# Kernel optimization log

Measured on AMD Instinct MI355X. Metric: run time of the kernel, lower is better.

## Reference

```python
import jax, jax.numpy as jnp
import numpy as np

N_KNOTS = 10
NEXPERTS = 1
NC = 8
STEP = 1.0 / (N_KNOTS - 1.0)
BN_EPS = 1e-5


def _spline_matrix(n, step):
    # natural cubic spline second-derivative solve matrix (precalc in torch code)
    mat = 4.0 * np.eye(n - 2)
    np.fill_diagonal(mat[1:, :-1], 1.0)
    np.fill_diagonal(mat[:-1, 1:], 1.0)
    A = 6.0 * np.linalg.inv(mat) / step ** 2
    z = np.zeros((1, n - 2))
    A = np.vstack([z, A, z])                      # [n, n-2]
    B = np.zeros((n - 2, n))
    np.fill_diagonal(B, 1.0)
    np.fill_diagonal(B[:, 1:], -2.0)
    np.fill_diagonal(B[:, 2:], 1.0)
    return jnp.asarray(A @ B, dtype=jnp.float32)  # [n, n]


def _conv(x, w, b, stride=2):
    y = jax.lax.conv_general_dilated(x, w, (stride, stride), 'VALID',
                                     dimension_numbers=('NCHW', 'OIHW', 'NCHW'))
    return y + b[None, :, None, None]


def _bn(x, g, be):
    # training-mode batchnorm (module default)
    m = x.mean(axis=(0, 2, 3), keepdims=True)
    v = x.var(axis=(0, 2, 3), keepdims=True)
    return g[None, :, None, None] * (x - m) * jax.lax.rsqrt(v + BN_EPS) + be[None, :, None, None]


def _interpolate(ys, mat):
    # ys: [..., n] -> cubic coeffs a,b,c,d each [..., n-1]
    h = STEP
    M = jnp.einsum('ij,...j->...i', mat, ys)
    a = (M[..., 1:] - M[..., :-1]) / (6.0 * h)
    b = M[..., :-1] / 2.0
    c = (ys[..., 1:] - ys[..., :-1]) / h - (M[..., 1:] + 2.0 * M[..., :-1]) * (h / 6.0)
    d = ys[..., :-1]
    return a, b, c, d


def _apply(coeffs, x):
    # coeffs: 4-tuple each [..., n-1]; x: [..., P] with matching leading dims
    a, b, c, d = coeffs
    xi = jnp.clip(jnp.floor(x / STEP), 0.0, N_KNOTS - 2.0)
    xf = x - xi * STEP
    idx = xi.astype(jnp.int32)
    ag = jnp.take_along_axis(a, idx, axis=-1)
    bg = jnp.take_along_axis(b, idx, axis=-1)
    cg = jnp.take_along_axis(c, idx, axis=-1)
    dg = jnp.take_along_axis(d, idx, axis=-1)
    return ((ag * xf + bg) * xf + cg) * xf + dg


def forward(x, w1, b1, w2, b2, g2, be2, w3, b3, g3, be3, w4, b4, g4, be4,
            w5, b5, g5, be5, fc1_w, fc1_b, fc2_w, fc2_b):
    B, C, H, W = x.shape
    small = x if (H, W) == (256, 256) else jax.image.resize(x, (B, C, 256, 256), 'bilinear')
    h = jax.nn.relu(_conv(small, w1, b1))
    h = _bn(jax.nn.relu(_conv(h, w2, b2)), g2, be2)
    h = _bn(jax.nn.relu(_conv(h, w3, b3)), g3, be3)
    h = _bn(jax.nn.relu(_conv(h, w4, b4)), g4, be4)
    h = _bn(jax.nn.relu(_conv(h, w5, b5)), g5, be5)   # [B, 16nc, 7, 7]
    h = h.mean(axis=(2, 3))                            # avgpool 7 -> [B, 16nc]
    h = jax.nn.relu(h @ fc1_w.T + fc1_b)
    ys = (h @ fc2_w.T + fc2_b).reshape(B, NEXPERTS, 3, N_KNOTS)
    identity = jnp.arange(N_KNOTS, dtype=jnp.float32) / (N_KNOTS - 1.0)
    ysn = ys + identity                                # residual spline
    mat = _spline_matrix(N_KNOTS, STEP)
    coeffs = _interpolate(ysn, mat)                    # each [B,E,3,n-1]
    # per-pixel spline eval at original resolution
    px = jnp.broadcast_to(x.reshape(B, 1, 3, H * W), (B, NEXPERTS, 3, H * W))
    out = _apply(coeffs, px).reshape(B, NEXPERTS, 3, H, W)
    out = jnp.transpose(out, (1, 0, 2, 3, 4))          # [E,B,3,H,W]
    # spline curves sampled at xs = arange(0,1,1/255) (255 points; detached in torch)
    xs = jnp.arange(0.0, 1.0, 1.0 / 255.0, dtype=jnp.float32)
    xs_b = jnp.broadcast_to(xs, (B, NEXPERTS, 3, xs.shape[0]))
    splines = jnp.transpose(_apply(coeffs, xs_b), (1, 0, 2, 3))  # [E,B,3,255]
    return out, splines


def setup_inputs() -> dict:
    key = jax.random.key(0)
    ks = jax.random.split(key, 16)
    n, nc, E = N_KNOTS, NC, NEXPERTS
    d = {}
    d['x'] = jax.random.uniform(ks[0], (8, 3, 1024, 1024), dtype=jnp.float32)
    d['w1'] = jax.random.normal(ks[1], (nc, 3, 3, 3), jnp.float32) * 0.1
    d['b1'] = jnp.zeros((nc,), jnp.float32)
    chans = [nc, 2 * nc, 4 * nc, 8 * nc, 16 * nc]
    for i, (ci, co) in enumerate(zip(chans[:-1], chans[1:]), start=2):
        d[f'w{i}'] = jax.random.normal(ks[i], (co, ci, 3, 3), jnp.float32) * 0.1
        d[f'b{i}'] = jnp.zeros((co,), jnp.float32)
        d[f'g{i}'] = jnp.ones((co,), jnp.float32)
        d[f'be{i}'] = jnp.zeros((co,), jnp.float32)
    d['fc1_w'] = jax.random.normal(ks[10], (16 * nc, 16 * nc), jnp.float32) * 0.05
    d['fc1_b'] = jnp.zeros((16 * nc,), jnp.float32)
    d['fc2_w'] = jax.random.normal(ks[11], (3 * n * E, 16 * nc), jnp.float32) * 0.05
    d['fc2_b'] = jnp.zeros((3 * n * E,), jnp.float32)
    return d


def reference(x, w1, b1, w2, b2, g2, be2, w3, b3, g3, be3, w4, b4, g4, be4,
              w5, b5, g5, be5, fc1_w, fc1_b, fc2_w, fc2_b):
    return forward(x, w1, b1, w2, b2, g2, be2, w3, b3, g3, be3, w4, b4, g4, be4,
                   w5, b5, g5, be5, fc1_w, fc1_b, fc2_w, fc2_b)
```

## Files before the change

kernel.cpp:

```cpp
#include <hip/hip_runtime.h>

#define SPLINE_OFF 25165824
#define STEP_F (1.0f/9.0f)

typedef float f32x4 __attribute__((ext_vector_type(4)));

__global__ __launch_bounds__(256) void resize_k(const float* __restrict__ x,
                                                float* __restrict__ sm) {
    __shared__ float vs[2][1024];
    const int blk = blockIdx.x;
    const int plane = blk >> 7;
    const int orA = (blk & 127) * 2;
    const int t = threadIdx.x;

    const float W[8] = {0.125f,0.375f,0.625f,0.875f,0.875f,0.625f,0.375f,0.125f};
    const float* p = x + (size_t)plane * 1048576 + t * 4;
    const int rA = 4 * orA - 2;

    float a0x=0.f,a0y=0.f,a0z=0.f,a0w=0.f;
    float a1x=0.f,a1y=0.f,a1z=0.f,a1w=0.f;

    if (rA >= 0 && rA + 11 <= 1023) {
        #pragma unroll
        for (int k = 0; k < 12; k++) {
            const float4 v = *(const float4*)(p + (size_t)(rA + k) * 1024);
            if (k < 8) {
                const float w = W[k] * 0.25f;
                a0x = fmaf(v.x, w, a0x); a0y = fmaf(v.y, w, a0y);
                a0z = fmaf(v.z, w, a0z); a0w = fmaf(v.w, w, a0w);
            }
            if (k >= 4) {
                const float w = W[k - 4] * 0.25f;
                a1x = fmaf(v.x, w, a1x); a1y = fmaf(v.y, w, a1y);
                a1z = fmaf(v.z, w, a1z); a1w = fmaf(v.w, w, a1w);
            }
        }
    } else {
        #pragma unroll
        for (int o = 0; o < 2; o++) {
            const int r0 = 4 * (orA + o) - 2;
            float bx=0.f,by=0.f,bz=0.f,bw=0.f,wsum=0.f;
            #pragma unroll
            for (int k = 0; k < 8; k++) {
                const int r = r0 + k;
                if (r >= 0 && r < 1024) {
                    const float4 v = *(const float4*)(p + (size_t)r * 1024);
                    bx = fmaf(v.x, W[k], bx); by = fmaf(v.y, W[k], by);
                    bz = fmaf(v.z, W[k], bz); bw = fmaf(v.w, W[k], bw);
                    wsum += W[k];
                }
            }
            const float inv = 1.f / wsum;
            if (o == 0) { a0x=bx*inv; a0y=by*inv; a0z=bz*inv; a0w=bw*inv; }
            else        { a1x=bx*inv; a1y=by*inv; a1z=bz*inv; a1w=bw*inv; }
        }
    }
    vs[0][4*t+0]=a0x; vs[0][4*t+1]=a0y; vs[0][4*t+2]=a0z; vs[0][4*t+3]=a0w;
    vs[1][4*t+0]=a1x; vs[1][4*t+1]=a1y; vs[1][4*t+2]=a1z; vs[1][4*t+3]=a1w;
    __syncthreads();

    const int c0 = 4 * t - 2;
    #pragma unroll
    for (int o = 0; o < 2; o++) {
        float acc = 0.f;
        if (c0 >= 0 && c0 + 7 <= 1023) {
            #pragma unroll
            for (int k = 0; k < 8; k++)
                acc = fmaf(vs[o][c0 + k], W[k] * 0.25f, acc);
        } else {
            float wsum = 0.f;
            #pragma unroll
            for (int k = 0; k < 8; k++) {
                const int c = c0 + k;
                if (c >= 0 && c < 1024) { acc = fmaf(vs[o][c], W[k], acc); wsum += W[k]; }
            }
            acc /= wsum;
        }
        sm[((size_t)plane * 256 + orA + o) * 256 + t] = acc;
    }
}

__global__ __launch_bounds__(256) void c1c2_k(
    const float* __restrict__ sm,
    const float* __restrict__ w1, const float* __restrict__ b1,
    const float* __restrict__ w2, const float* __restrict__ b2,
    float* __restrict__ h2, float* __restrict__ pS2, float* __restrict__ pQ2)
{
    __shared__ float smT[3 * 1225];
    __shared__ float c1T[8 * 289];
    __shared__ float w1s[216];
    __shared__ float w2s[1152];
    __shared__ float bs[24];

    const int tile = blockIdx.x;
    const int b    = blockIdx.y;
    const int tx = tile & 7, ty = tile >> 3;
    const int R0 = ty * 8, C0 = tx * 8;
    const int t = threadIdx.x;

    if (t < 216) w1s[t] = w1[t];
    for (int i = t; i < 1152; i += 256) w2s[i] = w2[i];
    if (t < 8) bs[t] = b1[t];
    else if (t < 24) bs[t] = b2[t - 8];

    const int r0 = 4 * R0, c0 = 4 * C0;
    for (int i = t; i < 3675; i += 256) {
        const int ch = i / 1225, rem = i - ch * 1225;
        const int r = rem / 35, c = rem - r * 35;
        const int gr = r0 + r, gc = c0 + c;
        float v = 0.f;
        if (gr < 256 && gc < 256)
            v = sm[((size_t)(b * 3 + ch) << 16) + (gr << 8) + gc];
        smT[i] = v;
    }
    __syncthreads();

    for (int i = t; i < 2312; i += 256) {
        const int co = i / 289, pp = i - co * 289;
        const int r = pp / 17, c = pp - r * 17;
        float acc = bs[co];
        #pragma unroll
        for (int ch = 0; ch < 3; ch++) {
            const float* sp = &smT[ch * 1225 + (2 * r) * 35 + 2 * c];
            const float* wp = &w1s[co * 27 + ch * 9];
            #pragma unroll
            for (int kh = 0; kh < 3; kh++) {
                acc = fmaf(sp[kh * 35 + 0], wp[kh * 3 + 0], acc);
                acc = fmaf(sp[kh * 35 + 1], wp[kh * 3 + 1], acc);
                acc = fmaf(sp[kh * 35 + 2], wp[kh * 3 + 2], acc);
            }
        }
        c1T[i] = fmaxf(acc, 0.f);
    }
    __syncthreads();

    const int px = t & 63, cog = t >> 6;
    const int pr = px >> 3, pc = px & 7;
    const bool valid = (R0 + pr < 63) && (C0 + pc < 63);
    float vals[4];
    #pragma unroll
    for (int k = 0; k < 4; k++) {
        const int co = cog * 4 + k;
        float acc = bs[8 + co];
        #pragma unroll
        for (int ci = 0; ci < 8; ci++) {
            const float* cp = &c1T[ci * 289 + (2 * pr) * 17 + 2 * pc];
            const float* wp = &w2s[co * 72 + ci * 9];
            #pragma unroll
            for (int kh = 0; kh < 3; kh++) {
                acc = fmaf(cp[kh * 17 + 0], wp[kh * 3 + 0], acc);
                acc = fmaf(cp[kh * 17 + 1], wp[kh * 3 + 1], acc);
                acc = fmaf(cp[kh * 17 + 2], wp[kh * 3 + 2], acc);
            }
        }
        const float v = valid ? fmaxf(acc, 0.f) : 0.f;
        vals[k] = v;
        if (valid)
            h2[(size_t)(b * 16 + co) * 3969 + (R0 + pr) * 63 + (C0 + pc)] = v;
    }
    #pragma unroll
    for (int k = 0; k < 4; k++) {
        float s = vals[k], q = vals[k] * vals[k];
        #pragma unroll
        for (int off = 32; off > 0; off >>= 1) {
            s += __shfl_down(s, off);
            q += __shfl_down(q, off);
        }
        if (px == 0) {
            const int co = cog * 4 + k;
            pS2[(b * 16 + co) * 64 + tile] = s;
            pQ2[(b * 16 + co) * 64 + tile] = q;
        }
    }
}

template<int CIN, int COUT, int INW, int OUTW, int CISPLIT, int PIX,
         int NTPREV, int NTOUT, bool INBN, bool STATS, bool WRITE>
__global__ __launch_bounds__(PIX * CISPLIT) void conv_k(
    const float* __restrict__ in, const float* __restrict__ w,
    const float* __restrict__ bias,
    const float* __restrict__ gam, const float* __restrict__ be,
    const float* __restrict__ pS, const float* __restrict__ pQ, float invN,
    float* __restrict__ out,
    float* __restrict__ pSo, float* __restrict__ pQo)
{
    constexpr int BLOCK = PIX * CISPLIT;
    constexpr int CPS = CIN / CISPLIT;
    constexpr int COG = COUT / 2;

    __shared__ float wsm[2][CIN * 9];
    __shared__ float scs[CIN], shs[CIN];
    __shared__ float wrow[2][CIN];
    __shared__ float cadd[2];
    __shared__ float part[CISPLIT][PIX][2];
    __shared__ float red[2][2][PIX / 64];
    __shared__ float sredS[BLOCK], sredQ[BLOCK];

    const int tid = threadIdx.x;
    const int p   = tid & (PIX - 1);
    const int cs  = tid / PIX;
    const int bc  = blockIdx.y;
    const int b   = bc / COG;
    const int co0 = (bc % COG) * 2;

    if constexpr (INBN) {
        constexpr int GRP = BLOCK / CIN;
        constexpr int TERMS = 8 * NTPREV;
        const int ci = tid % CIN;
        const int gi = tid / CIN;
        float s = 0.f, q = 0.f;
        for (int j = gi; j < TERMS; j += GRP) {
            const int bb = j / NTPREV, tl = j - bb * NTPREV;
            const int a = (bb * CIN + ci) * NTPREV + tl;
            s += pS[a]; q += pQ[a];
        }
        sredS[gi * CIN + ci] = s;
        sredQ[gi * CIN + ci] = q;
        __syncthreads();
        if (tid < CIN) {
            float ts = 0.f, tq = 0.f;
            #pragma unroll
            for (int g2 = 0; g2 < GRP; g2++) {
                ts += sredS[g2 * CIN + tid];
                tq += sredQ[g2 * CIN + tid];
            }
            const float m = ts * invN;
            const float v = tq * invN - m * m;
            const float sc = gam[tid] * rsqrtf(v + 1e-5f);
            scs[tid] = sc;
            shs[tid] = be[tid] - m * sc;
        }
        __syncthreads();
    }

    for (int i = tid; i < 2 * CIN * 9; i += BLOCK) {
        const int n = i / (CIN * 9), r = i - n * (CIN * 9), ci = r / 9;
        const float wv = w[(co0 + n) * CIN * 9 + r];
        wsm[n][r] = INBN ? wv * scs[ci] : wv;
    }
    if constexpr (INBN) {
        for (int i = tid; i < 2 * CIN; i += BLOCK) {
            const int n = i / CIN, ci = i - n * CIN;
            const float* wp = w + ((co0 + n) * CIN + ci) * 9;
            float s = 0.f;
            #pragma unroll
            for (int k = 0; k < 9; k++) s += wp[k];
            wrow[n][ci] = s;
        }
    }
    __syncthreads();
    if (tid < 2) {
        float c = bias[co0 + tid];
        if constexpr (INBN) {
            for (int ci = 0; ci < CIN; ci++) c = fmaf(wrow[tid][ci], shs[ci], c);
        }
        cadd[tid] = c;
    }
    __syncthreads();

    const int npix = OUTW * OUTW;
    const int pg = blockIdx.x * PIX + p;
    float a0 = 0.f, a1 = 0.f;
    if (pg < npix) {
        const int oh = pg / OUTW, ow = pg - oh * OUTW;
        const float* ib = in + ((size_t)(b * CIN) + cs * CPS) * (INW * INW)
                             + (size_t)(2 * oh) * INW + 2 * ow;
        #pragma unroll 4
        for (int ci = 0; ci < CPS; ci++) {
            const float* ip = ib + (size_t)ci * (INW * INW);
            const int cw = (cs * CPS + ci) * 9;
            #pragma unroll
            for (int kh = 0; kh < 3; kh++) {
                const float* r = ip + kh * INW;
                #pragma unroll
                for (int kw = 0; kw < 3; kw++) {
                    const float xv = r[kw];
                    a0 = fmaf(xv, wsm[0][cw + kh * 3 + kw], a0);
                    a1 = fmaf(xv, wsm[1][cw + kh * 3 + kw], a1);
                }
            }
        }
    }

    float v0 = 0.f, v1 = 0.f;
    if constexpr (CISPLIT > 1) {
        part[cs][p][0] = a0; part[cs][p][1] = a1;
        __syncthreads();
    }
    if (cs == 0) {
        float s0 = a0, s1 = a1;
        if constexpr (CISPLIT > 1) {
            #pragma unroll
            for (int q = 1; q < CISPLIT; q++) { s0 += part[q][p][0]; s1 += part[q][p][1]; }
        }
        if (pg < npix) {
            v0 = fmaxf(s0 + cadd[0], 0.f);
            v1 = fmaxf(s1 + cadd[1], 0.f);
            if constexpr (WRITE) {
                out[(size_t)(b * COUT + co0) * npix + pg] = v0;
                out[(size_t)(b * COUT + co0 + 1) * npix + pg] = v1;
            }
        }
    }

    if constexpr (STATS) {
        if (cs == 0) {
            float sA = v0, qA = v0 * v0, sB = v1, qB = v1 * v1;
            #pragma unroll
            for (int off = 32; off > 0; off >>= 1) {
                sA += __shfl_down(sA, off); qA += __shfl_down(qA, off);
                sB += __shfl_down(sB, off); qB += __shfl_down(qB, off);
            }
            if ((tid & 63) == 0) {
                red[0][0][tid >> 6] = sA; red[0][1][tid >> 6] = qA;
                red[1][0][tid >> 6] = sB; red[1][1][tid >> 6] = qB;
            }
        }
        __syncthreads();
        if (tid == 0) {
            float tsA = 0.f, tqA = 0.f, tsB = 0.f, tqB = 0.f;
            #pragma unroll
            for (int i = 0; i < PIX / 64; i++) {
                tsA += red[0][0][i]; tqA += red[0][1][i];
                tsB += red[1][0][i]; tqB += red[1][1][i];
            }
            pSo[(b * COUT + co0) * NTOUT + blockIdx.x] = tsA;
            pQo[(b * COUT + co0) * NTOUT + blockIdx.x] = tqA;
            pSo[(b * COUT + co0 + 1) * NTOUT + blockIdx.x] = tsB;
            pQo[(b * COUT + co0 + 1) * NTOUT + blockIdx.x] = tqB;
        }
    }
}

__global__ __launch_bounds__(256) void fc_spline_k(
    const float* __restrict__ pS5, const float* __restrict__ pQ5,
    const float* __restrict__ g5, const float* __restrict__ be5,
    const float* __restrict__ fc1w, const float* __restrict__ fc1b,
    const float* __restrict__ fc2w, const float* __restrict__ fc2b,
    float* __restrict__ coeff_out, float* __restrict__ splines_out)
{
    __shared__ float sc5[128], sh5[128];
    __shared__ float h[1024];
    __shared__ float h1v[1024];
    __shared__ float ysn[240];
    __shared__ float coef[24][36];

    const int t = threadIdx.x;

    if (t < 128) {
        float s = 0.f, q = 0.f;
        #pragma unroll
        for (int b = 0; b < 8; b++) { s += pS5[b * 128 + t]; q += pQ5[b * 128 + t]; }
        float m = s * (1.f / 392.f);
        float v = q * (1.f / 392.f) - m * m;
        float sc = g5[t] * rsqrtf(v + 1e-5f);
        sc5[t] = sc;
        sh5[t] = be5[t] - m * sc;
    }
    __syncthreads();

    for (int i = t; i < 1024; i += 256) {
        int c = i & 127;
        h[i] = fmaf(sc5[c], pS5[i] * (1.f / 49.f), sh5[c]);
    }
    __syncthreads();

    for (int i = t; i < 1024; i += 256) {
        int b = i >> 7, j = i & 127;
        float acc = fc1b[j];
        for (int c = 0; c < 128; c++)
            acc = fmaf(h[(b << 7) + c], fc1w[(j << 7) + c], acc);
        h1v[i] = fmaxf(acc, 0.f);
    }
    __syncthreads();

    if (t < 240) {
        int b = t / 30, k = t % 30;
        float acc = fc2b[k];
        for (int j = 0; j < 128; j++)
            acc = fmaf(h1v[(b << 7) + j], fc2w[(k << 7) + j], acc);
        ysn[t] = acc + (float)(k % 10) * STEP_F;
    }
    __syncthreads();

    if (t < 24) {
        float y[10];
        #pragma unroll
        for (int i = 0; i < 10; i++) y[i] = ysn[t * 10 + i];
        float rhs[9], cp[9], dp[9];
        #pragma unroll
        for (int i = 1; i <= 8; i++)
            rhs[i] = 486.f * (y[i - 1] - 2.f * y[i] + y[i + 1]);
        cp[1] = 0.25f; dp[1] = rhs[1] * 0.25f;
        #pragma unroll
        for (int i = 2; i <= 8; i++) {
            float m = 1.f / (4.f - cp[i - 1]);
            cp[i] = m;
            dp[i] = (rhs[i] - dp[i - 1]) * m;
        }
        float M[10];
        M[0] = 0.f; M[9] = 0.f;
        M[8] = dp[8];
        #pragma unroll
        for (int i = 7; i >= 1; i--) M[i] = dp[i] - cp[i] * M[i + 1];
        #pragma unroll
        for (int i = 0; i < 9; i++) {
            float a = (M[i + 1] - M[i]) * 1.5f;
            float bb = M[i] * 0.5f;
            float cc = (y[i + 1] - y[i]) * 9.f - (M[i + 1] + 2.f * M[i]) * (STEP_F / 6.f);
            float dd = y[i];
            coef[t][i] = a; coef[t][9 + i] = bb; coef[t][18 + i] = cc; coef[t][27 + i] = dd;
            coeff_out[t * 36 + i] = a;
            coeff_out[t * 36 + 9 + i] = bb;
            coeff_out[t * 36 + 18 + i] = cc;
            coeff_out[t * 36 + 27 + i] = dd;
        }
    }
    __syncthreads();

    for (int i = t; i < 24 * 255; i += 256) {
        int bc = i / 255, k = i - bc * 255;
        float xv = (float)k * (1.0f / 255.0f);
        float xi = floorf(xv * 9.0f);
        xi = fminf(fmaxf(xi, 0.f), 8.f);
        int ix = (int)xi;
        float xf = xv - xi * STEP_F;
        const float* cf = coef[bc];
        splines_out[i] = fmaf(fmaf(fmaf(cf[ix], xf, cf[9 + ix]), xf, cf[18 + ix]), xf, cf[27 + ix]);
    }
}

__global__ __launch_bounds__(256) void apply_k(const float* __restrict__ x,
                                               const float* __restrict__ coeff,
                                               float* __restrict__ out)
{
    __shared__ float cf[36];
    const int blk = blockIdx.x;
    const int plane = blk >> 10;
    const int t = threadIdx.x;
    if (t < 36) cf[t] = coeff[plane * 36 + t];
    __syncthreads();

    size_t base = (size_t)blk * 1024 + (size_t)t * 4;
    float4 v = *(const float4*)(x + base);
    f32x4 o;
    #pragma unroll
    for (int k = 0; k < 4; k++) {
        float xv = (k == 0) ? v.x : (k == 1) ? v.y : (k == 2) ? v.z : v.w;
        float xi = floorf(xv * 9.0f);
        xi = fminf(fmaxf(xi, 0.f), 8.f);
        int ix = (int)xi;
        float xf = xv - xi * STEP_F;
        o[k] = fmaf(fmaf(fmaf(cf[ix], xf, cf[9 + ix]), xf, cf[18 + ix]), xf, cf[27 + ix]);
    }
    __builtin_nontemporal_store(o, (f32x4*)(out + base));
}

extern "C" void kernel_launch(void* const* d_in, const int* in_sizes, int n_in,
                              void* d_out, int out_size, void* d_ws, size_t ws_size,
                              hipStream_t stream) {
    (void)in_sizes; (void)n_in; (void)out_size; (void)ws_size;

    const float* x    = (const float*)d_in[0];
    const float* w1   = (const float*)d_in[1];
    const float* b1   = (const float*)d_in[2];
    const float* w2   = (const float*)d_in[3];
    const float* b2   = (const float*)d_in[4];
    const float* g2   = (const float*)d_in[5];
    const float* be2  = (const float*)d_in[6];
    const float* w3   = (const float*)d_in[7];
    const float* b3   = (const float*)d_in[8];
    const float* g3   = (const float*)d_in[9];
    const float* be3  = (const float*)d_in[10];
    const float* w4   = (const float*)d_in[11];
    const float* b4   = (const float*)d_in[12];
    const float* g4   = (const float*)d_in[13];
    const float* be4  = (const float*)d_in[14];
    const float* w5   = (const float*)d_in[15];
    const float* b5   = (const float*)d_in[16];
    const float* g5   = (const float*)d_in[17];
    const float* be5  = (const float*)d_in[18];
    const float* fc1w = (const float*)d_in[19];
    const float* fc1b = (const float*)d_in[20];
    const float* fc2w = (const float*)d_in[21];
    const float* fc2b = (const float*)d_in[22];

    float* out = (float*)d_out;
    float* wsf = (float*)d_ws;

    float* pS2 = wsf + 0;
    float* pQ2 = wsf + 8192;
    float* pS3 = wsf + 16384;
    float* pQ3 = wsf + 17408;
    float* pS4 = wsf + 18432;
    float* pQ4 = wsf + 18944;
    float* pS5 = wsf + 19456;
    float* pQ5 = wsf + 20480;
    float* coeff = wsf + 21504;

    float* sm  = out;
    float* h2  = out + 1572864;
    float* h3  = out + 2080896;
    float* h4  = out + 2326912;

    resize_k<<<3072, 256, 0, stream>>>(x, sm);

    c1c2_k<<<dim3(64, 8), 256, 0, stream>>>(sm, w1, b1, w2, b2, h2, pS2, pQ2);

    conv_k<16, 32, 63, 31, 2, 256, 64, 4, true, true, true>
        <<<dim3(4, 128), 512, 0, stream>>>(h2, w3, b3, g2, be2,
                                           pS2, pQ2, 1.0f / 31752.0f,
                                           h3, pS3, pQ3);
    conv_k<32, 64, 31, 15, 4, 256, 4, 1, true, true, true>
        <<<dim3(1, 256), 1024, 0, stream>>>(h3, w4, b4, g3, be3,
                                            pS3, pQ3, 1.0f / 7688.0f,
                                            h4, pS4, pQ4);
    conv_k<64, 128, 15, 7, 8, 64, 1, 1, true, true, false>
        <<<dim3(1, 512), 512, 0, stream>>>(h4, w5, b5, g4, be4,
                                           pS4, pQ4, 1.0f / 1800.0f,
                                           nullptr, pS5, pQ5);

    fc_spline_k<<<1, 256, 0, stream>>>(pS5, pQ5, g5, be5,
                                       fc1w, fc1b, fc2w, fc2b,
                                       coeff, out + SPLINE_OFF);

    apply_k<<<24576, 256, 0, stream>>>(x, coeff, out);
}
```

Baseline: 145.1 us.

## Restructure pipeline: split c1c2, fuse conv5 with FC/spline via atomic last-block

Result: faster. 130.5 us (median of 2 runs) (-10.0%).

```diff
diff --git a/kernel.cpp b/kernel.cpp
--- a/kernel.cpp
+++ b/kernel.cpp
@@ -6,38 +6,44 @@
 typedef float f32x4 __attribute__((ext_vector_type(4)));
 
 __global__ __launch_bounds__(256) void resize_k(const float* __restrict__ x,
-                                                float* __restrict__ sm) {
-    __shared__ float vs[2][1024];
+                                                float* __restrict__ sm,
+                                                unsigned* __restrict__ ctr) {
+    __shared__ float vs[4][1024];
     const int blk = blockIdx.x;
-    const int plane = blk >> 7;
-    const int orA = (blk & 127) * 2;
+    const int plane = blk >> 6;
+    const int orA = (blk & 63) * 4;
     const int t = threadIdx.x;
+    if (blk == 0 && t == 0) ctr[0] = 0u;
 
     const float W[8] = {0.125f,0.375f,0.625f,0.875f,0.875f,0.625f,0.375f,0.125f};
     const float* p = x + (size_t)plane * 1048576 + t * 4;
-    const int rA = 4 * orA - 2;
-
-    float a0x=0.f,a0y=0.f,a0z=0.f,a0w=0.f;
-    float a1x=0.f,a1y=0.f,a1z=0.f,a1w=0.f;
-
-    if (rA >= 0 && rA + 11 <= 1023) {
-        #pragma unroll
-        for (int k = 0; k < 12; k++) {
-            const float4 v = *(const float4*)(p + (size_t)(rA + k) * 1024);
-            if (k < 8) {
-                const float w = W[k] * 0.25f;
-                a0x = fmaf(v.x, w, a0x); a0y = fmaf(v.y, w, a0y);
-                a0z = fmaf(v.z, w, a0z); a0w = fmaf(v.w, w, a0w);
-            }
-            if (k >= 4) {
-                const float w = W[k - 4] * 0.25f;
-                a1x = fmaf(v.x, w, a1x); a1y = fmaf(v.y, w, a1y);
-                a1z = fmaf(v.z, w, a1z); a1w = fmaf(v.w, w, a1w);
+    const int rb = 4 * orA - 2;
+
+    float acc[4][4];
+    #pragma unroll
+    for (int o = 0; o < 4; o++)
+        #pragma unroll
+        for (int c = 0; c < 4; c++) acc[o][c] = 0.f;
+
+    if (rb >= 0 && rb + 19 <= 1023) {
+        #pragma unroll
+        for (int k = 0; k < 20; k++) {
+            const float4 v = *(const float4*)(p + (size_t)(rb + k) * 1024);
+            #pragma unroll
+            for (int o = 0; o < 4; o++) {
+                const int j = k - 4 * o;
+                if (j >= 0 && j < 8) {
+                    const float w = W[j] * 0.25f;
+                    acc[o][0] = fmaf(v.x, w, acc[o][0]);
+                    acc[o][1] = fmaf(v.y, w, acc[o][1]);
+                    acc[o][2] = fmaf(v.z, w, acc[o][2]);
+                    acc[o][3] = fmaf(v.w, w, acc[o][3]);
+                }
             }
         }
     } else {
         #pragma unroll
-        for (int o = 0; o < 2; o++) {
+        for (int o = 0; o < 4; o++) {
             const int r0 = 4 * (orA + o) - 2;
             float bx=0.f,by=0.f,bz=0.f,bw=0.f,wsum=0.f;
             #pragma unroll
@@ -51,126 +57,34 @@
                 }
             }
             const float inv = 1.f / wsum;
-            if (o == 0) { a0x=bx*inv; a0y=by*inv; a0z=bz*inv; a0w=bw*inv; }
-            else        { a1x=bx*inv; a1y=by*inv; a1z=bz*inv; a1w=bw*inv; }
-        }
-    }
-    vs[0][4*t+0]=a0x; vs[0][4*t+1]=a0y; vs[0][4*t+2]=a0z; vs[0][4*t+3]=a0w;
-    vs[1][4*t+0]=a1x; vs[1][4*t+1]=a1y; vs[1][4*t+2]=a1z; vs[1][4*t+3]=a1w;
+            acc[o][0]=bx*inv; acc[o][1]=by*inv; acc[o][2]=bz*inv; acc[o][3]=bw*inv;
+        }
+    }
+    #pragma unroll
+    for (int o = 0; o < 4; o++) {
+        vs[o][4*t+0]=acc[o][0]; vs[o][4*t+1]=acc[o][1];
+        vs[o][4*t+2]=acc[o][2]; vs[o][4*t+3]=acc[o][3];
+    }
     __syncthreads();
 
     const int c0 = 4 * t - 2;
     #pragma unroll
-    for (int o = 0; o < 2; o++) {
-        float acc = 0.f;
+    for (int o = 0; o < 4; o++) {
+        float a = 0.f;
         if (c0 >= 0 && c0 + 7 <= 1023) {
             #pragma unroll
             for (int k = 0; k < 8; k++)
-                acc = fmaf(vs[o][c0 + k], W[k] * 0.25f, acc);
+                a = fmaf(vs[o][c0 + k], W[k] * 0.25f, a);
         } else {
             float wsum = 0.f;
             #pragma unroll
             for (int k = 0; k < 8; k++) {
                 const int c = c0 + k;
-                if (c >= 0 && c < 1024) { acc = fmaf(vs[o][c], W[k], acc); wsum += W[k]; }
-            }
-            acc /= wsum;
-        }
-        sm[((size_t)plane * 256 + orA + o) * 256 + t] = acc;
-    }
-}
-
-__global__ __launch_bounds__(256) void c1c2_k(
-    const float* __restrict__ sm,
-    const float* __restrict__ w1, const float* __restrict__ b1,
-    const float* __restrict__ w2, const float* __restrict__ b2,
-    float* __restrict__ h2, float* __restrict__ pS2, float* __restrict__ pQ2)
-{
-    __shared__ float smT[3 * 1225];
-    __shared__ float c1T[8 * 289];
-    __shared__ float w1s[216];
-    __shared__ float w2s[1152];
-    __shared__ float bs[24];
-
-    const int tile = blockIdx.x;
-    const int b    = blockIdx.y;
-    const int tx = tile & 7, ty = tile >> 3;
-    const int R0 = ty * 8, C0 = tx * 8;
-    const int t = threadIdx.x;
-
-    if (t < 216) w1s[t] = w1[t];
-    for (int i = t; i < 1152; i += 256) w2s[i] = w2[i];
-    if (t < 8) bs[t] = b1[t];
-    else if (t < 24) bs[t] = b2[t - 8];
-
-    const int r0 = 4 * R0, c0 = 4 * C0;
-    for (int i = t; i < 3675; i += 256) {
-        const int ch = i / 1225, rem = i - ch * 1225;
-        const int r = rem / 35, c = rem - r * 35;
-        const int gr = r0 + r, gc = c0 + c;
-        float v = 0.f;
-        if (gr < 256 && gc < 256)
-            v = sm[((size_t)(b * 3 + ch) << 16) + (gr << 8) + gc];
-        smT[i] = v;
-    }
-    __syncthreads();
-
-    for (int i = t; i < 2312; i += 256) {
-        const int co = i / 289, pp = i - co * 289;
-        const int r = pp / 17, c = pp - r * 17;
-        float acc = bs[co];
-        #pragma unroll
-        for (int ch = 0; ch < 3; ch++) {
-            const float* sp = &smT[ch * 1225 + (2 * r) * 35 + 2 * c];
-            const float* wp = &w1s[co * 27 + ch * 9];
-            #pragma unroll
-            for (int kh = 0; kh < 3; kh++) {
-                acc = fmaf(sp[kh * 35 + 0], wp[kh * 3 + 0], acc);
-                acc = fmaf(sp[kh * 35 + 1], wp[kh * 3 + 1], acc);
-                acc = fmaf(sp[kh * 35 + 2], wp[kh * 3 + 2], acc);
-            }
-        }
-        c1T[i] = fmaxf(acc, 0.f);
-    }
-    __syncthreads();
-
-    const int px = t & 63, cog = t >> 6;
-    const int pr = px >> 3, pc = px & 7;
-    const bool valid = (R0 + pr < 63) && (C0 + pc < 63);
-    float vals[4];
-    #pragma unroll
-    for (int k = 0; k < 4; k++) {
-        const int co = cog * 4 + k;
-        float acc = bs[8 + co];
-        #pragma unroll
-        for (int ci = 0; ci < 8; ci++) {
-            const float* cp = &c1T[ci * 289 + (2 * pr) * 17 + 2 * pc];
-            const float* wp = &w2s[co * 72 + ci * 9];
-            #pragma unroll
-            for (int kh = 0; kh < 3; kh++) {
-                acc = fmaf(cp[kh * 17 + 0], wp[kh * 3 + 0], acc);
-                acc = fmaf(cp[kh * 17 + 1], wp[kh * 3 + 1], acc);
-                acc = fmaf(cp[kh * 17 + 2], wp[kh * 3 + 2], acc);
-            }
-        }
-        const float v = valid ? fmaxf(acc, 0.f) : 0.f;
-        vals[k] = v;
-        if (valid)
-            h2[(size_t)(b * 16 + co) * 3969 + (R0 + pr) * 63 + (C0 + pc)] = v;
-    }
-    #pragma unroll
-    for (int k = 0; k < 4; k++) {
-        float s = vals[k], q = vals[k] * vals[k];
-        #pragma unroll
-        for (int off = 32; off > 0; off >>= 1) {
-            s += __shfl_down(s, off);
-            q += __shfl_down(q, off);
-        }
-        if (px == 0) {
-            const int co = cog * 4 + k;
-            pS2[(b * 16 + co) * 64 + tile] = s;
-            pQ2[(b * 16 + co) * 64 + tile] = q;
-        }
+                if (c >= 0 && c < 1024) { a = fmaf(vs[o][c], W[k], a); wsum += W[k]; }
+            }
+            a /= wsum;
+        }
+        sm[((size_t)plane * 256 + orA + o) * 256 + t] = a;
     }
 }
 
@@ -332,61 +246,188 @@
     }
 }
 
-__global__ __launch_bounds__(256) void fc_spline_k(
-    const float* __restrict__ pS5, const float* __restrict__ pQ5,
+__global__ __launch_bounds__(256) void conv5fc_k(
+    const float* __restrict__ in, const float* __restrict__ w,
+    const float* __restrict__ bias,
+    const float* __restrict__ gam, const float* __restrict__ be,
+    const float* __restrict__ pS, const float* __restrict__ pQ,
+    float* __restrict__ pS5, float* __restrict__ pQ5,
     const float* __restrict__ g5, const float* __restrict__ be5,
     const float* __restrict__ fc1w, const float* __restrict__ fc1b,
     const float* __restrict__ fc2w, const float* __restrict__ fc2b,
-    float* __restrict__ coeff_out, float* __restrict__ splines_out)
+    float* __restrict__ coeff_out, float* __restrict__ splines_out,
+    unsigned* __restrict__ ctr)
 {
-    __shared__ float sc5[128], sh5[128];
-    __shared__ float h[1024];
-    __shared__ float h1v[1024];
-    __shared__ float ysn[240];
-    __shared__ float coef[24][36];
-
-    const int t = threadIdx.x;
-
+    constexpr int CIN = 64, COUT = 128, INW = 15, OUTW = 7;
+    constexpr int CISPLIT = 4, PIX = 64, BLOCK = 256;
+    constexpr int CPS = CIN / CISPLIT;
+    constexpr int COG = COUT / 2;
+    const float invN = 1.0f / 1800.0f;
+
+    __shared__ float wsm[2][CIN * 9];
+    __shared__ float scs[CIN], shs[CIN];
+    __shared__ float wrow[2][CIN];
+    __shared__ float cadd[2];
+    __shared__ float part[CISPLIT][PIX][2];
+    __shared__ float sredS[BLOCK], sredQ[BLOCK];
+    __shared__ unsigned lastFlag;
+    __shared__ float fsc5[128], fsh5[128];
+    __shared__ float fch[1024], fh1[1024];
+    __shared__ float fysn[240];
+    __shared__ float fcoef[24][36];
+
+    const int tid = threadIdx.x;
+    const int p   = tid & (PIX - 1);
+    const int cs  = tid / PIX;
+    const int bc  = blockIdx.x;
+    const int b   = bc / COG;
+    const int co0 = (bc % COG) * 2;
+
+    {
+        constexpr int GRP = BLOCK / CIN;
+        const int ci = tid % CIN;
+        const int gi = tid / CIN;
+        float s = 0.f, q = 0.f;
+        for (int j = gi; j < 8; j += GRP) {
+            const int a = j * CIN + ci;
+            s += pS[a]; q += pQ[a];
+        }
+        sredS[gi * CIN + ci] = s;
+        sredQ[gi * CIN + ci] = q;
+        __syncthreads();
+        if (tid < CIN) {
+            float ts = 0.f, tq = 0.f;
+            #pragma unroll
+            for (int g2 = 0; g2 < GRP; g2++) {
+                ts += sredS[g2 * CIN + tid];
+                tq += sredQ[g2 * CIN + tid];
+            }
+            const float m = ts * invN;
+            const float v = tq * invN - m * m;
+            const float sc = gam[tid] * rsqrtf(v + 1e-5f);
+            scs[tid] = sc;
+            shs[tid] = be[tid] - m * sc;
+        }
+        __syncthreads();
+    }
+
+    for (int i = tid; i < 2 * CIN * 9; i += BLOCK) {
+        const int n = i / (CIN * 9), r = i - n * (CIN * 9), ci = r / 9;
+        wsm[n][r] = w[(co0 + n) * CIN * 9 + r] * scs[ci];
+    }
+    for (int i = tid; i < 2 * CIN; i += BLOCK) {
+        const int n = i / CIN, ci = i - n * CIN;
+        const float* wp = w + ((co0 + n) * CIN + ci) * 9;
+        float s = 0.f;
+        #pragma unroll
+        for (int k = 0; k < 9; k++) s += wp[k];
+        wrow[n][ci] = s;
+    }
+    __syncthreads();
+    if (tid < 2) {
+        float c = bias[co0 + tid];
+        for (int ci = 0; ci < CIN; ci++) c = fmaf(wrow[tid][ci], shs[ci], c);
+        cadd[tid] = c;
+    }
+    __syncthreads();
+
+    float a0 = 0.f, a1 = 0.f;
+    if (p < 49) {
+        const int oh = p / OUTW, ow = p - oh * OUTW;
+        const float* ib = in + ((size_t)(b * CIN) + cs * CPS) * (INW * INW)
+                             + (size_t)(2 * oh) * INW + 2 * ow;
+        #pragma unroll 4
+        for (int ci = 0; ci < CPS; ci++) {
+            const float* ip = ib + (size_t)ci * (INW * INW);
+            const int cw = (cs * CPS + ci) * 9;
+            #pragma unroll
+            for (int kh = 0; kh < 3; kh++) {
+                const float* r = ip + kh * INW;
+                #pragma unroll
+                for (int kw = 0; kw < 3; kw++) {
+                    const float xv = r[kw];
+                    a0 = fmaf(xv, wsm[0][cw + kh * 3 + kw], a0);
+                    a1 = fmaf(xv, wsm[1][cw + kh * 3 + kw], a1);
+                }
+            }
+        }
+    }
+
+    part[cs][p][0] = a0; part[cs][p][1] = a1;
+    __syncthreads();
+    if (cs == 0) {
+        float s0 = a0 + part[1][p][0] + part[2][p][0] + part[3][p][0];
+        float s1 = a1 + part[1][p][1] + part[2][p][1] + part[3][p][1];
+        float v0 = 0.f, v1 = 0.f;
+        if (p < 49) {
+            v0 = fmaxf(s0 + cadd[0], 0.f);
+            v1 = fmaxf(s1 + cadd[1], 0.f);
+        }
+        float sA = v0, qA = v0 * v0, sB = v1, qB = v1 * v1;
+        #pragma unroll
+        for (int off = 32; off > 0; off >>= 1) {
+            sA += __shfl_down(sA, off); qA += __shfl_down(qA, off);
+            sB += __shfl_down(sB, off); qB += __shfl_down(qB, off);
+        }
+        if (p == 0) {
+            pS5[b * COUT + co0] = sA;
+            pQ5[b * COUT + co0] = qA;
+            pS5[b * COUT + co0 + 1] = sB;
+            pQ5[b * COUT + co0 + 1] = qB;
+        }
+    }
+    __syncthreads();
+
+    if (tid == 0) {
+        __threadfence();
+        unsigned old = atomicAdd(ctr, 1u);
+        lastFlag = (old == 511u) ? 1u : 0u;
+    }
+    __syncthreads();
+    if (lastFlag == 0u) return;
+    __threadfence();
+
+    const int t = tid;
     if (t < 128) {
-        float s = 0.f, q = 0.f;
-        #pragma unroll
-        for (int b = 0; b < 8; b++) { s += pS5[b * 128 + t]; q += pQ5[b * 128 + t]; }
-        float m = s * (1.f / 392.f);
-        float v = q * (1.f / 392.f) - m * m;
+        float sv = 0.f, qv = 0.f;
+        #pragma unroll
+        for (int bb = 0; bb < 8; bb++) { sv += pS5[bb * 128 + t]; qv += pQ5[bb * 128 + t]; }
+        float m = sv * (1.f / 392.f);
+        float v = qv * (1.f / 392.f) - m * m;
         float sc = g5[t] * rsqrtf(v + 1e-5f);
-        sc5[t] = sc;
-        sh5[t] = be5[t] - m * sc;
+        fsc5[t] = sc;
+        fsh5[t] = be5[t] - m * sc;
     }
     __syncthreads();
 
     for (int i = t; i < 1024; i += 256) {
         int c = i & 127;
-        h[i] = fmaf(sc5[c], pS5[i] * (1.f / 49.f), sh5[c]);
+        fch[i] = fmaf(fsc5[c], pS5[i] * (1.f / 49.f), fsh5[c]);
     }
     __syncthreads();
 
     for (int i = t; i < 1024; i += 256) {
-        int b = i >> 7, j = i & 127;
+        int bb = i >> 7, j = i & 127;
         float acc = fc1b[j];
         for (int c = 0; c < 128; c++)
-            acc = fmaf(h[(b << 7) + c], fc1w[(j << 7) + c], acc);
-        h1v[i] = fmaxf(acc, 0.f);
+            acc = fmaf(fch[(bb << 7) + c], fc1w[(j << 7) + c], acc);
+        fh1[i] = fmaxf(acc, 0.f);
     }
     __syncthreads();
 
     if (t < 240) {
-        int b = t / 30, k = t % 30;
+        int bb = t / 30, k = t % 30;
         float acc = fc2b[k];
         for (int j = 0; j < 128; j++)
-            acc = fmaf(h1v[(b << 7) + j], fc2w[(k << 7) + j], acc);
-        ysn[t] = acc + (float)(k % 10) * STEP_F;
+            acc = fmaf(fh1[(bb << 7) + j], fc2w[(k << 7) + j], acc);
+        fysn[t] = acc + (float)(k % 10) * STEP_F;
     }
     __syncthreads();
 
     if (t < 24) {
         float y[10];
         #pragma unroll
-        for (int i = 0; i < 10; i++) y[i] = ysn[t * 10 + i];
+        for (int i = 0; i < 10; i++) y[i] = fysn[t * 10 + i];
         float rhs[9], cp[9], dp[9];
         #pragma unroll
         for (int i = 1; i <= 8; i++)
@@ -406,12 +447,12 @@
         #pragma unroll
         for (int i = 0; i < 9; i++) {
             float a = (M[i + 1] - M[i]) * 1.5f;
-            float bb = M[i] * 0.5f;
+            float bb2 = M[i] * 0.5f;
             float cc = (y[i + 1] - y[i]) * 9.f - (M[i + 1] + 2.f * M[i]) * (STEP_F / 6.f);
             float dd = y[i];
-            coef[t][i] = a; coef[t][9 + i] = bb; coef[t][18 + i] = cc; coef[t][27 + i] = dd;
+            fcoef[t][i] = a; fcoef[t][9 + i] = bb2; fcoef[t][18 + i] = cc; fcoef[t][27 + i] = dd;
             coeff_out[t * 36 + i] = a;
-            coeff_out[t * 36 + 9 + i] = bb;
+            coeff_out[t * 36 + 9 + i] = bb2;
             coeff_out[t * 36 + 18 + i] = cc;
             coeff_out[t * 36 + 27 + i] = dd;
         }
@@ -419,13 +460,13 @@
     __syncthreads();
 
     for (int i = t; i < 24 * 255; i += 256) {
-        int bc = i / 255, k = i - bc * 255;
+        int bc2 = i / 255, k = i - bc2 * 255;
         float xv = (float)k * (1.0f / 255.0f);
         float xi = floorf(xv * 9.0f);
         xi = fminf(fmaxf(xi, 0.f), 8.f);
         int ix = (int)xi;
         float xf = xv - xi * STEP_F;
-        const float* cf = coef[bc];
+        const float* cf = fcoef[bc2];
         splines_out[i] = fmaf(fmaf(fmaf(cf[ix], xf, cf[9 + ix]), xf, cf[18 + ix]), xf, cf[27 + ix]);
     }
 }
@@ -489,40 +530,44 @@
     float* wsf = (float*)d_ws;
 
     float* pS2 = wsf + 0;
-    float* pQ2 = wsf + 8192;
-    float* pS3 = wsf + 16384;
-    float* pQ3 = wsf + 17408;
-    float* pS4 = wsf + 18432;
-    float* pQ4 = wsf + 18944;
-    float* pS5 = wsf + 19456;
-    float* pQ5 = wsf + 20480;
-    float* coeff = wsf + 21504;
+    float* pQ2 = wsf + 2048;
+    float* pS3 = wsf + 4096;
+    float* pQ3 = wsf + 5120;
+    float* pS4 = wsf + 6144;
+    float* pQ4 = wsf + 6656;
+    float* pS5 = wsf + 7168;
+    float* pQ5 = wsf + 8192;
+    float* coeff = wsf + 9216;
+    unsigned* ctr = (unsigned*)(wsf + 10240);
 
     float* sm  = out;
-    float* h2  = out + 1572864;
-    float* h3  = out + 2080896;
-    float* h4  = out + 2326912;
-
-    resize_k<<<3072, 256, 0, stream>>>(x, sm);
-
-    c1c2_k<<<dim3(64, 8), 256, 0, stream>>>(sm, w1, b1, w2, b2, h2, pS2, pQ2);
-
-    conv_k<16, 32, 63, 31, 2, 256, 64, 4, true, true, true>
-        <<<dim3(4, 128), 512, 0, stream>>>(h2, w3, b3, g2, be2,
+    float* h1  = out + 1572864;
+    float* h2  = out + 2605120;
+    float* h3  = out + 3113152;
+    float* h4  = out + 3359168;
+
+    resize_k<<<1536, 256, 0, stream>>>(x, sm, ctr);
+
+    conv_k<3, 8, 256, 127, 1, 256, 1, 1, false, false, true>
+        <<<dim3(64, 32), 256, 0, stream>>>(sm, w1, b1, nullptr, nullptr,
+                                           nullptr, nullptr, 0.f,
+                                           h1, nullptr, nullptr);
+    conv_k<8, 16, 127, 63, 1, 256, 1, 16, false, true, true>
+        <<<dim3(16, 64), 256, 0, stream>>>(h1, w2, b2, nullptr, nullptr,
+                                           nullptr, nullptr, 0.f,
+                                           h2, pS2, pQ2);
+    conv_k<16, 32, 63, 31, 1, 256, 16, 4, true, true, true>
+        <<<dim3(4, 128), 256, 0, stream>>>(h2, w3, b3, g2, be2,
                                            pS2, pQ2, 1.0f / 31752.0f,
                                            h3, pS3, pQ3);
-    conv_k<32, 64, 31, 15, 4, 256, 4, 1, true, true, true>
-        <<<dim3(1, 256), 1024, 0, stream>>>(h3, w4, b4, g3, be3,
-                                            pS3, pQ3, 1.0f / 7688.0f,
-                                            h4, pS4, pQ4);
-    conv_k<64, 128, 15, 7, 8, 64, 1, 1, true, true, false>
-        <<<dim3(1, 512), 512, 0, stream>>>(h4, w5, b5, g4, be4,
-                                           pS4, pQ4, 1.0f / 1800.0f,
-                                           nullptr, pS5, pQ5);
-
-    fc_spline_k<<<1, 256, 0, stream>>>(pS5, pQ5, g5, be5,
-                                       fc1w, fc1b, fc2w, fc2b,
-                                       coeff, out + SPLINE_OFF);
+    conv_k<32, 64, 31, 15, 2, 256, 4, 1, true, true, true>
+        <<<dim3(1, 256), 512, 0, stream>>>(h3, w4, b4, g3, be3,
+                                           pS3, pQ3, 1.0f / 7688.0f,
+                                           h4, pS4, pQ4);
+    conv5fc_k<<<512, 256, 0, stream>>>(h4, w5, b5, g4, be4,
+                                       pS4, pQ4, pS5, pQ5,
+                                       g5, be5, fc1w, fc1b, fc2w, fc2b,
+                                       coeff, out + SPLINE_OFF, ctr);
 
     apply_k<<<24576, 256, 0, stream>>>(x, coeff, out);
 }
```
